# Optimization experiments

Hardware: AMD Instinct MI355X
Metric: run time of the kernel (lower is better)

Reference implementation:

```python
import jax, jax.numpy as jnp
import numpy as np

N_NODE = 200000
EMB = 64
N_EDGES = 2000000
LAYERS = 3
EPS_NORM = 1e-12


def setup_inputs() -> dict:
    key = jax.random.key(0)
    ks = jax.random.split(key, 13)
    d = EMB
    return {
        "user_emb": jax.random.normal(ks[0], (N_NODE, d), jnp.float32),
        "W0": jax.random.normal(ks[1], (d, d), jnp.float32) * np.float32(np.sqrt(2.0 / d)),
        "b0": jax.random.normal(ks[2], (1, d), jnp.float32) * 0.1,
        "W1": jax.random.normal(ks[3], (d, d), jnp.float32) * np.float32(np.sqrt(2.0 / d)),
        "b1": jax.random.normal(ks[4], (1, d), jnp.float32) * 0.1,
        "att": jax.random.normal(ks[5], (1, d), jnp.float32) * 0.1,
        "att_m": jax.random.normal(ks[6], (d, d), jnp.float32) * np.float32(np.sqrt(2.0 / d)),
        "item_rows": jax.random.randint(ks[7], (N_EDGES,), 0, N_NODE, jnp.int32),
        "item_cols": jax.random.randint(ks[8], (N_EDGES,), 0, N_NODE, jnp.int32),
        "item_vals": jax.random.uniform(ks[9], (N_EDGES,), jnp.float32),
        "user_rows": jax.random.randint(ks[10], (N_EDGES,), 0, N_NODE, jnp.int32),
        "user_cols": jax.random.randint(ks[11], (N_EDGES,), 0, N_NODE, jnp.int32),
        "user_vals": jax.random.uniform(ks[12], (N_EDGES,), jnp.float32),
    }


def _spmm(rows, cols, vals, x):
    # y[i] = sum_{edges (i,j)} vals * x[j]   (torch.sparse.mm equivalent)
    gathered = vals[:, None] * x[cols]  # [E, d]
    return jax.ops.segment_sum(gathered, rows, num_segments=N_NODE)


def _l2norm_rows(x):
    # F.normalize(x, p=2, dim=1)
    n = jnp.sqrt(jnp.sum(x * x, axis=1, keepdims=True))
    return x / jnp.maximum(n, EPS_NORM)


def _self_gating(em, W, b):
    return em * jax.nn.sigmoid(em @ W + b)


def _propagate(rows, cols, vals, u):
    acc = u
    for _ in range(LAYERS):
        u = _spmm(rows, cols, vals, u)
        acc = acc + _l2norm_rows(u)
    return acc


def reference(user_emb, W0, b0, W1, b1, att, att_m,
              item_rows, item_cols, item_vals,
              user_rows, user_cols, user_vals):
    u_c2 = _self_gating(user_emb, W0, b0)
    u_c3 = _self_gating(user_emb, W1, b1)
    e2 = _propagate(item_rows, item_cols, item_vals, u_c2)  # [N, d]
    e3 = _propagate(user_rows, user_cols, user_vals, u_c3)  # [N, d]
    # channel attention: per-node scalar score for each channel
    w2 = jnp.sum(att * (e2 @ att_m), axis=1)  # [N]
    w3 = jnp.sum(att * (e3 @ att_m), axis=1)  # [N]
    score = jax.nn.softmax(jnp.stack([w2, w3], axis=1), axis=-1)  # [N, 2]
    mixed = score[:, 0:1] * e2 + score[:, 1:2] * e3  # [N, d]
    return mixed, score
```

## Files before the change

kernel.cpp:

```cpp
#include <hip/hip_runtime.h>

#define N_NODE 200000
#define EMB 64
#define N_EDGES 2000000
#define NROWS_TOTAL (2 * N_NODE)
#define TOT_E (2 * N_EDGES)

#define BSHIFT 9
#define BROWS 512
#define NBUCK ((NROWS_TOTAL + BROWS - 1) / BROWS)
#define NB 1024
#define CHUNK ((TOT_E + NB - 1) / NB)
#define SCAN_N (NBUCK * NB)
#define MAXH 6144

typedef unsigned short bfu;
typedef __attribute__((ext_vector_type(8))) short bf16x8;
typedef __attribute__((ext_vector_type(4))) float f32x4;

__device__ __forceinline__ float bf2f(bfu u) { return __uint_as_float(((unsigned)u) << 16); }
__device__ __forceinline__ bfu f2bf(float f) {
    unsigned b = __float_as_uint(f);
    return (bfu)((b + 0x7FFF + ((b >> 16) & 1)) >> 16);
}

__global__ void gate_kernel(const float* __restrict__ emb,
                            const float* __restrict__ W,
                            const float* __restrict__ b,
                            bfu* __restrict__ out, int n) {
    int t = threadIdx.x;
    int w = t >> 6, lane = t & 63;
    int l16 = lane & 15, kg = lane >> 4;
    bf16x8 Bf[2][4];
#pragma unroll
    for (int kb = 0; kb < 2; ++kb)
#pragma unroll
        for (int nt = 0; nt < 4; ++nt) {
            bf16x8 f;
#pragma unroll
            for (int e = 0; e < 8; ++e)
                f[e] = (short)f2bf(W[(kb * 32 + kg * 8 + e) * 64 + nt * 16 + l16]);
            Bf[kb][nt] = f;
        }
    float bias[4];
#pragma unroll
    for (int nt = 0; nt < 4; ++nt) bias[nt] = b[nt * 16 + l16];
    const float4* e4 = (const float4*)emb;
#pragma unroll 1
    for (int it = 0; it < 4; ++it) {
        int tile = blockIdx.x * 16 + w * 4 + it;
        if (tile * 16 >= n) break;
        int arow = tile * 16 + l16;
        size_t ab = (size_t)arow * 16 + kg * 2;
        float4 a0 = e4[ab], a1 = e4[ab + 1];
        float4 a2 = e4[ab + 8], a3 = e4[ab + 9];
        bf16x8 A0, A1;
        A0[0] = (short)f2bf(a0.x); A0[1] = (short)f2bf(a0.y);
        A0[2] = (short)f2bf(a0.z); A0[3] = (short)f2bf(a0.w);
        A0[4] = (short)f2bf(a1.x); A0[5] = (short)f2bf(a1.y);
        A0[6] = (short)f2bf(a1.z); A0[7] = (short)f2bf(a1.w);
        A1[0] = (short)f2bf(a2.x); A1[1] = (short)f2bf(a2.y);
        A1[2] = (short)f2bf(a2.z); A1[3] = (short)f2bf(a2.w);
        A1[4] = (short)f2bf(a3.x); A1[5] = (short)f2bf(a3.y);
        A1[6] = (short)f2bf(a3.z); A1[7] = (short)f2bf(a3.w);
        f32x4 acc[4];
#pragma unroll
        for (int nt = 0; nt < 4; ++nt) {
            acc[nt] = (f32x4){0.f, 0.f, 0.f, 0.f};
            acc[nt] = __builtin_amdgcn_mfma_f32_16x16x32_bf16(A0, Bf[0][nt], acc[nt], 0, 0, 0);
            acc[nt] = __builtin_amdgcn_mfma_f32_16x16x32_bf16(A1, Bf[1][nt], acc[nt], 0, 0, 0);
        }
#pragma unroll
        for (int nt = 0; nt < 4; ++nt) {
#pragma unroll
            for (int r = 0; r < 4; ++r) {
                int orow = tile * 16 + kg * 4 + r;
                int col = nt * 16 + l16;
                float s = acc[nt][r] + bias[nt];
                float g = 1.0f / (1.0f + __expf(-s));
                float xv = emb[(size_t)orow * 64 + col];
                out[(size_t)orow * 64 + col] = f2bf(xv * g);
            }
        }
    }
}

__global__ void binA_kernel(const int* __restrict__ item_rows,
                            const int* __restrict__ user_rows,
                            int* __restrict__ bc) {
    __shared__ int h[NBUCK];
    int t = threadIdx.x, blk = blockIdx.x;
    for (int k = t; k < NBUCK; k += 256) h[k] = 0;
    __syncthreads();
    int lo = blk * CHUNK, hi = min(lo + CHUNK, TOT_E);
    for (int i = lo + t; i < hi; i += 256) {
        int g = (i < N_EDGES) ? item_rows[i] : (N_NODE + user_rows[i - N_EDGES]);
        atomicAdd(&h[g >> BSHIFT], 1);
    }
    __syncthreads();
    for (int k = t; k < NBUCK; k += 256) bc[k * NB + blk] = h[k];
}

__global__ void scan1_kernel(const int* __restrict__ bc, int* __restrict__ bsumP,
                             int* __restrict__ btot) {
    int b = blockIdx.x, t = threadIdx.x;
    int base = b * NB + t * 4;
    int sR = 0, sP = 0;
#pragma unroll
    for (int k = 0; k < 4; ++k) {
        int c = bc[base + k];
        sR += c;
        sP += (c + 7) & ~7;
    }
#pragma unroll
    for (int off = 32; off; off >>= 1) {
        sR += __shfl_xor(sR, off);
        sP += __shfl_xor(sP, off);
    }
    __shared__ int wsR[4], wsP[4];
    int lane = t & 63, w = t >> 6;
    if (lane == 0) { wsR[w] = sR; wsP[w] = sP; }
    __syncthreads();
    if (t == 0) {
        btot[b] = wsR[0] + wsR[1] + wsR[2] + wsR[3];
        bsumP[b] = wsP[0] + wsP[1] + wsP[2] + wsP[3];
    }
}

__global__ void scan2_kernel(const int* __restrict__ bsumP, const int* __restrict__ btot,
                             int* __restrict__ boffP, int* __restrict__ bbase) {
    __shared__ int sh[1024];
    int t = threadIdx.x;
    int vP = (t < NBUCK) ? bsumP[t] : 0;
    sh[t] = vP;
    __syncthreads();
    for (int off = 1; off < 1024; off <<= 1) {
        int u = (t >= off) ? sh[t - off] : 0;
        __syncthreads();
        sh[t] += u;
        __syncthreads();
    }
    if (t < NBUCK) boffP[t] = sh[t] - vP;
    if (t == 1023) boffP[NBUCK] = sh[1023];
    __syncthreads();
    int vR = (t < NBUCK) ? btot[t] : 0;
    sh[t] = vR;
    __syncthreads();
    for (int off = 1; off < 1024; off <<= 1) {
        int u = (t >= off) ? sh[t - off] : 0;
        __syncthreads();
        sh[t] += u;
        __syncthreads();
    }
    if (t < NBUCK) bbase[t] = sh[t] - vR;
}

__global__ void scan3_kernel(const int* __restrict__ bc, const int* __restrict__ boffP,
                             int* __restrict__ soffP) {
    int b = blockIdx.x, t = threadIdx.x;
    int lane = t & 63, w = t >> 6;
    int base = b * NB + t * 4;
    int p[4];
#pragma unroll
    for (int k = 0; k < 4; ++k) p[k] = (bc[base + k] + 7) & ~7;
    int e1 = p[0], e2 = p[0] + p[1], e3 = p[0] + p[1] + p[2];
    int tsum = e3 + p[3];
    int incl = tsum;
#pragma unroll
    for (int off = 1; off < 64; off <<= 1) {
        int u = __shfl_up(incl, off);
        if (lane >= off) incl += u;
    }
    int excl = incl - tsum;
    __shared__ int wsum[4];
    if (lane == 63) wsum[w] = incl;
    __syncthreads();
    int woff = 0;
    for (int k = 0; k < 4; ++k) if (k < w) woff += wsum[k];
    int g = boffP[b] + woff + excl;
    soffP[base + 0] = g;
    soffP[base + 1] = g + e1;
    soffP[base + 2] = g + e2;
    soffP[base + 3] = g + e3;
}

__global__ void binB_kernel(const int* __restrict__ item_rows, const int* __restrict__ item_cols,
                            const float* __restrict__ item_vals,
                            const int* __restrict__ user_rows, const int* __restrict__ user_cols,
                            const float* __restrict__ user_vals,
                            const int* __restrict__ bc, const int* __restrict__ soffP,
                            int2* __restrict__ staged) {
    __shared__ int2 ebuf[CHUNK];
    __shared__ unsigned short sbk[CHUNK];
    __shared__ int lbase[NBUCK + 1];
    __shared__ int lcur[NBUCK];
    __shared__ int gb[NBUCK];
    __shared__ int wsum[4];
    int t = threadIdx.x, blk = blockIdx.x;
    for (int k = t; k < NBUCK; k += 256) gb[k] = soffP[k * NB + blk];
    {
        int i0 = t * 4;
        int p0 = (i0 < NBUCK) ? bc[i0 * NB + blk] : 0;
        int p1 = (i0 + 1 < NBUCK) ? bc[(i0 + 1) * NB + blk] : 0;
        int p2 = (i0 + 2 < NBUCK) ? bc[(i0 + 2) * NB + blk] : 0;
        int p3 = (i0 + 3 < NBUCK) ? bc[(i0 + 3) * NB + blk] : 0;
        int tsum = p0 + p1 + p2 + p3;
        int lane = t & 63, w = t >> 6;
        int incl = tsum;
#pragma unroll
        for (int off = 1; off < 64; off <<= 1) {
            int u = __shfl_up(incl, off);
            if (lane >= off) incl += u;
        }
        if (lane == 63) wsum[w] = incl;
        __syncthreads();
        int woff = 0;
        for (int k = 0; k < w; ++k) woff += wsum[k];
        int excl = woff + incl - tsum;
        if (i0 < NBUCK) { lbase[i0] = excl; lcur[i0] = excl; }
        if (i0 + 1 < NBUCK) { lbase[i0 + 1] = excl + p0; lcur[i0 + 1] = excl + p0; }
        if (i0 + 2 < NBUCK) { lbase[i0 + 2] = excl + p0 + p1; lcur[i0 + 2] = excl + p0 + p1; }
        if (i0 + 3 < NBUCK) { lbase[i0 + 3] = excl + p0 + p1 + p2; lcur[i0 + 3] = excl + p0 + p1 + p2; }
        if (t == 255) lbase[NBUCK] = excl + tsum;
    }
    __syncthreads();
    int lo = blk * CHUNK, hi = min(lo + CHUNK, TOT_E);
    int cnt = hi - lo;
    for (int i = lo + t; i < hi; i += 256) {
        int g, c; float v;
        if (i < N_EDGES) { g = item_rows[i]; c = item_cols[i]; v = item_vals[i]; }
        else { int j = i - N_EDGES; g = N_NODE + user_rows[j]; c = user_cols[j]; v = user_vals[j]; }
        int bk = g >> BSHIFT;
        int s = atomicAdd(&lcur[bk], 1);
        ebuf[s] = make_int2(((g & (BROWS - 1)) << 18) | c, __float_as_int(v));
        sbk[s] = (unsigned short)bk;
    }
    __syncthreads();
    for (int j = t; j < cnt; j += 256) {
        int k = sbk[j];
        staged[gb[k] + (j - lbase[k])] = ebuf[j];
    }
    for (int k = t; k < NBUCK; k += 256) {
        int c = lbase[k + 1] - lbase[k];
        int s = gb[k] + c, e = gb[k] + ((c + 7) & ~7);
        for (int q = s; q < e; ++q) staged[q] = make_int2(-1, 0);
    }
}

__global__ void finalize_kernel(const int2* __restrict__ staged, const int* __restrict__ boffP,
                                const int* __restrict__ bbase,
                                int* __restrict__ row_ptr, int2* __restrict__ ecv) {
    __shared__ int hist[BROWS];
    __shared__ int start[BROWS + 1];
    __shared__ int2 ebuf[MAXH];
    __shared__ int wsum[4];
    int b = blockIdx.x, t = threadIdx.x;
    int base = boffP[b], end = boffP[b + 1];
    int ebase = bbase[b];
    hist[t * 2] = 0; hist[t * 2 + 1] = 0;
    __syncthreads();
    for (int k = base + t; k < end; k += 256) {
        int gx = staged[k].x;
        if (gx >= 0) atomicAdd(&hist[gx >> 18], 1);
    }
    __syncthreads();
    int i0 = t * 2;
    int c0 = hist[i0], c1 = hist[i0 + 1];
    int tsum = c0 + c1;
    int lane = t & 63, w = t >> 6;
    int incl = tsum;
#pragma unroll
    for (int off = 1; off < 64; off <<= 1) {
        int u = __shfl_up(incl, off);
        if (lane >= off) incl += u;
    }
    if (lane == 63) wsum[w] = incl;
    __syncthreads();
    int woff = 0;
    for (int k = 0; k < w; ++k) woff += wsum[k];
    int excl = woff + incl - tsum;
    start[i0] = excl; start[i0 + 1] = excl + c0;
    if (t == 255) start[BROWS] = excl + tsum;
    __syncthreads();
    int tot = start[BROWS];
#pragma unroll
    for (int q = 0; q < 2; ++q) {
        int r = i0 + q;
        int g = (b << BSHIFT) + r;
        if (g < NROWS_TOTAL) row_ptr[g] = ebase + start[r];
    }
    if (b == 0 && t == 0) row_ptr[NROWS_TOTAL] = TOT_E;
    if (tot <= MAXH) {
        hist[i0] = start[i0]; hist[i0 + 1] = start[i0 + 1];
        __syncthreads();
        for (int k = base + t; k < end; k += 256) {
            int2 p = staged[k];
            if (p.x < 0) continue;
            int l = atomicAdd(&hist[p.x >> 18], 1);
            ebuf[l] = make_int2(p.x & 0x3FFFF, p.y);
        }
        __syncthreads();
        for (int j = t; j < tot; j += 256) ecv[ebase + j] = ebuf[j];
    } else {
        hist[i0] = ebase + start[i0]; hist[i0 + 1] = ebase + start[i0 + 1];
        __syncthreads();
        for (int k = base + t; k < end; k += 256) {
            int2 p = staged[k];
            if (p.x < 0) continue;
            int pos = atomicAdd(&hist[p.x >> 18], 1);
            ecv[pos] = make_int2(p.x & 0x3FFFF, p.y);
        }
    }
}

__global__ void spmm_y(const int* __restrict__ row_ptr, const int2* __restrict__ ecv,
                       const bfu* __restrict__ x,
                       bfu* __restrict__ y, float* __restrict__ rinv, int n) {
    int t = threadIdx.x;
    int lane = t & 63;
    int sub = lane >> 4;
    int l16 = lane & 15;
    int i = blockIdx.x * 16 + (t >> 6) * 4 + sub;
    if (i >= n) return;
    int s = row_ptr[i], e = row_ptr[i + 1];
    const ushort4* x4 = (const ushort4*)x;
    float4 a = make_float4(0.f, 0.f, 0.f, 0.f);
    int gbase = sub * 16;
    for (int base = s; base < e; base += 16) {
        int idx = base + l16;
        int cl = 0; float vl = 0.0f;
        if (idx < e) { int2 p = ecv[idx]; cl = p.x; vl = __int_as_float(p.y); }
        int cnt = min(16, e - base);
        int cnt4 = (cnt + 3) & ~3;
        for (int k = 0; k < cnt4; k += 4) {
#pragma unroll
            for (int u = 0; u < 4; ++u) {
                int c = __shfl(cl, gbase + k + u);
                float v = __shfl(vl, gbase + k + u);
                ushort4 xv = x4[(size_t)c * 16 + l16];
                a.x += v * bf2f(xv.x); a.y += v * bf2f(xv.y);
                a.z += v * bf2f(xv.z); a.w += v * bf2f(xv.w);
            }
        }
    }
    size_t o4 = (size_t)i * 16 + l16;
    ushort4 bv;
    bv.x = f2bf(a.x); bv.y = f2bf(a.y); bv.z = f2bf(a.z); bv.w = f2bf(a.w);
    ((ushort4*)y)[o4] = bv;
    float sq = a.x * a.x + a.y * a.y + a.z * a.z + a.w * a.w;
#pragma unroll
    for (int off = 8; off; off >>= 1) sq += __shfl_xor(sq, off);
    if (l16 == 0) rinv[i] = 1.0f / fmaxf(sqrtf(sq), 1e-12f);
}

__global__ void spmm_sum(const int* __restrict__ row_ptr, const int2* __restrict__ ecv,
                         const bfu* __restrict__ x ,
                         const bfu* __restrict__ u0, const bfu* __restrict__ y1,
                         const float* __restrict__ r1, const float* __restrict__ r2,
                         float* __restrict__ mixed, int n) {
    int t = threadIdx.x;
    int lane = t & 63;
    int sub = lane >> 4;
    int l16 = lane & 15;
    int i = blockIdx.x * 16 + (t >> 6) * 4 + sub;
    if (i >= n) return;
    int s = row_ptr[i], e = row_ptr[i + 1];
    const ushort4* x4 = (const ushort4*)x;
    float4 a = make_float4(0.f, 0.f, 0.f, 0.f);
    int gbase = sub * 16;
    for (int base = s; base < e; base += 16) {
        int idx = base + l16;
        int cl = 0; float vl = 0.0f;
        if (idx < e) { int2 p = ecv[idx]; cl = p.x; vl = __int_as_float(p.y); }
        int cnt = min(16, e - base);
        int cnt4 = (cnt + 3) & ~3;
        for (int k = 0; k < cnt4; k += 4) {
#pragma unroll
            for (int u = 0; u < 4; ++u) {
                int c = __shfl(cl, gbase + k + u);
                float v = __shfl(vl, gbase + k + u);
                ushort4 xv = x4[(size_t)c * 16 + l16];
                a.x += v * bf2f(xv.x); a.y += v * bf2f(xv.y);
                a.z += v * bf2f(xv.z); a.w += v * bf2f(xv.w);
            }
        }
    }
    float sq = a.x * a.x + a.y * a.y + a.z * a.z + a.w * a.w;
#pragma unroll
    for (int off = 8; off; off >>= 1) sq += __shfl_xor(sq, off);
    float r3 = 1.0f / fmaxf(sqrtf(sq), 1e-12f);
    size_t o4 = (size_t)i * 16 + l16;
    float a1 = r1[i], a2 = r2[i];
    ushort4 b0 = ((const ushort4*)u0)[o4];
    ushort4 b1 = ((const ushort4*)y1)[o4];
    ushort4 b2 = ((const ushort4*)x)[o4];
    float4 o;
    o.x = bf2f(b0.x) + a1 * bf2f(b1.x) + a2 * bf2f(b2.x) + r3 * a.x;
    o.y = bf2f(b0.y) + a1 * bf2f(b1.y) + a2 * bf2f(b2.y) + r3 * a.y;
    o.z = bf2f(b0.z) + a1 * bf2f(b1.z) + a2 * bf2f(b2.z) + r3 * a.z;
    o.w = bf2f(b0.w) + a1 * bf2f(b1.w) + a2 * bf2f(b2.w) + r3 * a.w;
    ((float4*)mixed)[o4] = o;
}

__global__ void spmm_mix(const int* __restrict__ row_ptr, const int2* __restrict__ ecv,
                         const bfu* __restrict__ x ,
                         const bfu* __restrict__ u0, const bfu* __restrict__ y1,
                         const float* __restrict__ r1, const float* __restrict__ r2,
                         float* __restrict__ mixed, const float* __restrict__ vvec,
                         float* __restrict__ score, int n) {
    int t = threadIdx.x;
    int lane = t & 63;
    int sub = lane >> 4;
    int l16 = lane & 15;
    int i = blockIdx.x * 16 + (t >> 6) * 4 + sub;
    if (i >= n) return;
    int s = row_ptr[i], e = row_ptr[i + 1];
    const ushort4* x4 = (const ushort4*)x;
    float4 a = make_float4(0.f, 0.f, 0.f, 0.f);
    int gbase = sub * 16;
    for (int base = s; base < e; base += 16) {
        int idx = base + l16;
        int cl = 0; float vl = 0.0f;
        if (idx < e) { int2 p = ecv[idx]; cl = p.x; vl = __int_as_float(p.y); }
        int cnt = min(16, e - base);
        int cnt4 = (cnt + 3) & ~3;
        for (int k = 0; k < cnt4; k += 4) {
#pragma unroll
            for (int u = 0; u < 4; ++u) {
                int c = __shfl(cl, gbase + k + u);
                float v = __shfl(vl, gbase + k + u);
                ushort4 xv = x4[(size_t)c * 16 + l16];
                a.x += v * bf2f(xv.x); a.y += v * bf2f(xv.y);
                a.z += v * bf2f(xv.z); a.w += v * bf2f(xv.w);
            }
        }
    }
    float sq = a.x * a.x + a.y * a.y + a.z * a.z + a.w * a.w;
#pragma unroll
    for (int off = 8; off; off >>= 1) sq += __shfl_xor(sq, off);
    float r3 = 1.0f / fmaxf(sqrtf(sq), 1e-12f);
    size_t o4 = (size_t)i * 16 + l16;
    float a1 = r1[i], a2s = r2[i];
    ushort4 b0 = ((const ushort4*)u0)[o4];
    ushort4 b1 = ((const ushort4*)y1)[o4];
    ushort4 b2 = ((const ushort4*)x)[o4];
    float4 a3;
    a3.x = bf2f(b0.x) + a1 * bf2f(b1.x) + a2s * bf2f(b2.x) + r3 * a.x;
    a3.y = bf2f(b0.y) + a1 * bf2f(b1.y) + a2s * bf2f(b2.y) + r3 * a.y;
    a3.z = bf2f(b0.z) + a1 * bf2f(b1.z) + a2s * bf2f(b2.z) + r3 * a.z;
    a3.w = bf2f(b0.w) + a1 * bf2f(b1.w) + a2s * bf2f(b2.w) + r3 * a.w;
    float4 a2 = ((float4*)mixed)[o4];
    float4 vv = ((const float4*)vvec)[l16];
    float w2 = a2.x * vv.x + a2.y * vv.y + a2.z * vv.z + a2.w * vv.w;
    float w3 = a3.x * vv.x + a3.y * vv.y + a3.z * vv.z + a3.w * vv.w;
#pragma unroll
    for (int off = 8; off; off >>= 1) {
        w2 += __shfl_xor(w2, off);
        w3 += __shfl_xor(w3, off);
    }
    float m = fmaxf(w2, w3);
    float x2 = __expf(w2 - m), x3 = __expf(w3 - m);
    float inv = 1.0f / (x2 + x3);
    float s2 = x2 * inv, s3 = x3 * inv;
    float4 o;
    o.x = s2 * a2.x + s3 * a3.x; o.y = s2 * a2.y + s3 * a3.y;
    o.z = s2 * a2.z + s3 * a3.z; o.w = s2 * a2.w + s3 * a3.w;
    ((float4*)mixed)[o4] = o;
    if (l16 == 0) { score[(size_t)i * 2] = s2; score[(size_t)i * 2 + 1] = s3; }
}

__global__ void vvec_kernel(const float* __restrict__ att_m, const float* __restrict__ att,
                            float* __restrict__ v) {
    int k = threadIdx.x;
    float s = 0.0f;
    for (int j = 0; j < 64; ++j) s += att_m[k * 64 + j] * att[j];
    v[k] = s;
}

extern "C" void kernel_launch(void* const* d_in, const int* in_sizes, int n_in,
                              void* d_out, int out_size, void* d_ws, size_t ws_size,
                              hipStream_t stream) {
    const float* user_emb = (const float*)d_in[0];
    const float* W0 = (const float*)d_in[1];
    const float* b0 = (const float*)d_in[2];
    const float* W1 = (const float*)d_in[3];
    const float* b1 = (const float*)d_in[4];
    const float* att = (const float*)d_in[5];
    const float* att_m = (const float*)d_in[6];
    const int* item_rows = (const int*)d_in[7];
    const int* item_cols = (const int*)d_in[8];
    const float* item_vals = (const float*)d_in[9];
    const int* user_rows = (const int*)d_in[10];
    const int* user_cols = (const int*)d_in[11];
    const float* user_vals = (const float*)d_in[12];

    float* out = (float*)d_out;
    float* mixed = out;
    float* score = out + (size_t)N_NODE * 64;

    char* w = (char*)d_ws;
    bfu* u0 = (bfu*)w;         w += (size_t)N_NODE * 64 * 2;
    bfu* y1 = (bfu*)w;         w += (size_t)N_NODE * 64 * 2;
    bfu* y2 = (bfu*)w;         w += (size_t)N_NODE * 64 * 2;
    float* rv1 = (float*)w;    w += (size_t)N_NODE * 4;
    float* rv2 = (float*)w;    w += (size_t)N_NODE * 4;
    int* row_ptr = (int*)w;    w += ((size_t)NROWS_TOTAL + 64) * 4;
    int2* ecv = (int2*)w;      w += (size_t)TOT_E * 8;
    float* vvec = (float*)w;   w += 256;
    int* bc = (int*)w;         w += (size_t)SCAN_N * 4;
    int* soffP = (int*)w;      w += (size_t)SCAN_N * 4;
    int* bsumP = (int*)w;      w += (NBUCK + 8) * 4;
    int* btot = (int*)w;       w += (NBUCK + 8) * 4;
    int* boffP = (int*)w;      w += (NBUCK + 8) * 4;
    int* bbase = (int*)w;      w += (NBUCK + 8) * 4;
    int2* staged = (int2*)u0;

    const int NB16 = (N_NODE + 15) / 16;
    const int GATE_B = (N_NODE / 16 + 15) / 16;
    const int* rp_item = row_ptr;
    const int* rp_user = row_ptr + N_NODE;

    binA_kernel<<<NB, 256, 0, stream>>>(item_rows, user_rows, bc);
    scan1_kernel<<<NBUCK, 256, 0, stream>>>(bc, bsumP, btot);
    scan2_kernel<<<1, 1024, 0, stream>>>(bsumP, btot, boffP, bbase);
    scan3_kernel<<<NBUCK, 256, 0, stream>>>(bc, boffP, soffP);
    binB_kernel<<<NB, 256, 0, stream>>>(item_rows, item_cols, item_vals,
                                        user_rows, user_cols, user_vals, bc, soffP, staged);
    finalize_kernel<<<NBUCK, 256, 0, stream>>>(staged, boffP, bbase, row_ptr, ecv);
    vvec_kernel<<<1, 64, 0, stream>>>(att_m, att, vvec);

    gate_kernel<<<GATE_B, 256, 0, stream>>>(user_emb, W0, b0, u0, N_NODE);
    spmm_y<<<NB16, 256, 0, stream>>>(rp_item, ecv, u0, y1, rv1, N_NODE);
    spmm_y<<<NB16, 256, 0, stream>>>(rp_item, ecv, y1, y2, rv2, N_NODE);
    spmm_sum<<<NB16, 256, 0, stream>>>(rp_item, ecv, y2, u0, y1, rv1, rv2, mixed, N_NODE);

    gate_kernel<<<GATE_B, 256, 0, stream>>>(user_emb, W1, b1, u0, N_NODE);
    spmm_y<<<NB16, 256, 0, stream>>>(rp_user, ecv, u0, y1, rv1, N_NODE);
    spmm_y<<<NB16, 256, 0, stream>>>(rp_user, ecv, y1, y2, rv2, N_NODE);
    spmm_mix<<<NB16, 256, 0, stream>>>(rp_user, ecv, y2, u0, y1, rv1, rv2,
                                       mixed, vvec, score, N_NODE);
}
```

Measured before the change: 438.5 us.

## Assign one wavefront per row and split edges across four lane groups in SpMM

The SpMM kernels now map one 64-lane wavefront to each row instead of one 16-lane group per row. The four 16-lane groups each process every fourth edge, and their partial sums are then reduced with cross-group shuffles. This shortens the serial chain of dependent gathers per row so more loads are in flight at once. In exchange it launches four times as many blocks, adds reduction shuffles, and leaves lanes idle on rows whose degree is not a multiple of four.

```diff
diff --git a/kernel.cpp b/kernel.cpp
--- a/kernel.cpp
+++ b/kernel.cpp
@@ -318,39 +318,35 @@
                        bfu* __restrict__ y, float* __restrict__ rinv, int n) {
     int t = threadIdx.x;
     int lane = t & 63;
-    int sub = lane >> 4;
+    int eg = lane >> 4;
     int l16 = lane & 15;
-    int i = blockIdx.x * 16 + (t >> 6) * 4 + sub;
+    int i = blockIdx.x * 4 + (t >> 6);
     if (i >= n) return;
     int s = row_ptr[i], e = row_ptr[i + 1];
     const ushort4* x4 = (const ushort4*)x;
     float4 a = make_float4(0.f, 0.f, 0.f, 0.f);
-    int gbase = sub * 16;
-    for (int base = s; base < e; base += 16) {
-        int idx = base + l16;
-        int cl = 0; float vl = 0.0f;
-        if (idx < e) { int2 p = ecv[idx]; cl = p.x; vl = __int_as_float(p.y); }
-        int cnt = min(16, e - base);
-        int cnt4 = (cnt + 3) & ~3;
-        for (int k = 0; k < cnt4; k += 4) {
-#pragma unroll
-            for (int u = 0; u < 4; ++u) {
-                int c = __shfl(cl, gbase + k + u);
-                float v = __shfl(vl, gbase + k + u);
-                ushort4 xv = x4[(size_t)c * 16 + l16];
-                a.x += v * bf2f(xv.x); a.y += v * bf2f(xv.y);
-                a.z += v * bf2f(xv.z); a.w += v * bf2f(xv.w);
-            }
-        }
-    }
-    size_t o4 = (size_t)i * 16 + l16;
-    ushort4 bv;
-    bv.x = f2bf(a.x); bv.y = f2bf(a.y); bv.z = f2bf(a.z); bv.w = f2bf(a.w);
-    ((ushort4*)y)[o4] = bv;
+    for (int base = s; base < e; base += 4) {
+        int idx = base + eg;
+        int c = 0; float v = 0.0f;
+        if (idx < e) { int2 p = ecv[idx]; c = p.x; v = __int_as_float(p.y); }
+        ushort4 xv = x4[(size_t)c * 16 + l16];
+        a.x += v * bf2f(xv.x); a.y += v * bf2f(xv.y);
+        a.z += v * bf2f(xv.z); a.w += v * bf2f(xv.w);
+    }
+#pragma unroll
+    for (int off = 16; off <= 32; off <<= 1) {
+        a.x += __shfl_xor(a.x, off); a.y += __shfl_xor(a.y, off);
+        a.z += __shfl_xor(a.z, off); a.w += __shfl_xor(a.w, off);
+    }
+    if (eg == 0) {
+        ushort4 bv;
+        bv.x = f2bf(a.x); bv.y = f2bf(a.y); bv.z = f2bf(a.z); bv.w = f2bf(a.w);
+        ((ushort4*)y)[(size_t)i * 16 + l16] = bv;
+    }
     float sq = a.x * a.x + a.y * a.y + a.z * a.z + a.w * a.w;
 #pragma unroll
-    for (int off = 8; off; off >>= 1) sq += __shfl_xor(sq, off);
-    if (l16 == 0) rinv[i] = 1.0f / fmaxf(sqrtf(sq), 1e-12f);
+    for (int off = 1; off <= 8; off <<= 1) sq += __shfl_xor(sq, off);
+    if (lane == 0) rinv[i] = 1.0f / fmaxf(sqrtf(sq), 1e-12f);
 }
 
 __global__ void spmm_sum(const int* __restrict__ row_ptr, const int2* __restrict__ ecv,
@@ -360,46 +356,43 @@
                          float* __restrict__ mixed, int n) {
     int t = threadIdx.x;
     int lane = t & 63;
-    int sub = lane >> 4;
+    int eg = lane >> 4;
     int l16 = lane & 15;
-    int i = blockIdx.x * 16 + (t >> 6) * 4 + sub;
+    int i = blockIdx.x * 4 + (t >> 6);
     if (i >= n) return;
     int s = row_ptr[i], e = row_ptr[i + 1];
     const ushort4* x4 = (const ushort4*)x;
     float4 a = make_float4(0.f, 0.f, 0.f, 0.f);
-    int gbase = sub * 16;
-    for (int base = s; base < e; base += 16) {
-        int idx = base + l16;
-        int cl = 0; float vl = 0.0f;
-        if (idx < e) { int2 p = ecv[idx]; cl = p.x; vl = __int_as_float(p.y); }
-        int cnt = min(16, e - base);
-        int cnt4 = (cnt + 3) & ~3;
-        for (int k = 0; k < cnt4; k += 4) {
-#pragma unroll
-            for (int u = 0; u < 4; ++u) {
-                int c = __shfl(cl, gbase + k + u);
-                float v = __shfl(vl, gbase + k + u);
-                ushort4 xv = x4[(size_t)c * 16 + l16];
-                a.x += v * bf2f(xv.x); a.y += v * bf2f(xv.y);
-                a.z += v * bf2f(xv.z); a.w += v * bf2f(xv.w);
-            }
-        }
+    for (int base = s; base < e; base += 4) {
+        int idx = base + eg;
+        int c = 0; float v = 0.0f;
+        if (idx < e) { int2 p = ecv[idx]; c = p.x; v = __int_as_float(p.y); }
+        ushort4 xv = x4[(size_t)c * 16 + l16];
+        a.x += v * bf2f(xv.x); a.y += v * bf2f(xv.y);
+        a.z += v * bf2f(xv.z); a.w += v * bf2f(xv.w);
+    }
+#pragma unroll
+    for (int off = 16; off <= 32; off <<= 1) {
+        a.x += __shfl_xor(a.x, off); a.y += __shfl_xor(a.y, off);
+        a.z += __shfl_xor(a.z, off); a.w += __shfl_xor(a.w, off);
     }
     float sq = a.x * a.x + a.y * a.y + a.z * a.z + a.w * a.w;
 #pragma unroll
-    for (int off = 8; off; off >>= 1) sq += __shfl_xor(sq, off);
-    float r3 = 1.0f / fmaxf(sqrtf(sq), 1e-12f);
-    size_t o4 = (size_t)i * 16 + l16;
-    float a1 = r1[i], a2 = r2[i];
-    ushort4 b0 = ((const ushort4*)u0)[o4];
-    ushort4 b1 = ((const ushort4*)y1)[o4];
-    ushort4 b2 = ((const ushort4*)x)[o4];
-    float4 o;
-    o.x = bf2f(b0.x) + a1 * bf2f(b1.x) + a2 * bf2f(b2.x) + r3 * a.x;
-    o.y = bf2f(b0.y) + a1 * bf2f(b1.y) + a2 * bf2f(b2.y) + r3 * a.y;
-    o.z = bf2f(b0.z) + a1 * bf2f(b1.z) + a2 * bf2f(b2.z) + r3 * a.z;
-    o.w = bf2f(b0.w) + a1 * bf2f(b1.w) + a2 * bf2f(b2.w) + r3 * a.w;
-    ((float4*)mixed)[o4] = o;
+    for (int off = 1; off <= 8; off <<= 1) sq += __shfl_xor(sq, off);
+    if (eg == 0) {
+        float r3 = 1.0f / fmaxf(sqrtf(sq), 1e-12f);
+        size_t o4 = (size_t)i * 16 + l16;
+        float a1 = r1[i], a2 = r2[i];
+        ushort4 b0 = ((const ushort4*)u0)[o4];
+        ushort4 b1 = ((const ushort4*)y1)[o4];
+        ushort4 b2 = ((const ushort4*)x)[o4];
+        float4 o;
+        o.x = bf2f(b0.x) + a1 * bf2f(b1.x) + a2 * bf2f(b2.x) + r3 * a.x;
+        o.y = bf2f(b0.y) + a1 * bf2f(b1.y) + a2 * bf2f(b2.y) + r3 * a.y;
+        o.z = bf2f(b0.z) + a1 * bf2f(b1.z) + a2 * bf2f(b2.z) + r3 * a.z;
+        o.w = bf2f(b0.w) + a1 * bf2f(b1.w) + a2 * bf2f(b2.w) + r3 * a.w;
+        ((float4*)mixed)[o4] = o;
+    }
 }
 
 __global__ void spmm_mix(const int* __restrict__ row_ptr, const int2* __restrict__ ecv,
@@ -410,34 +403,29 @@
                          float* __restrict__ score, int n) {
     int t = threadIdx.x;
     int lane = t & 63;
-    int sub = lane >> 4;
+    int eg = lane >> 4;
     int l16 = lane & 15;
-    int i = blockIdx.x * 16 + (t >> 6) * 4 + sub;
+    int i = blockIdx.x * 4 + (t >> 6);
     if (i >= n) return;
     int s = row_ptr[i], e = row_ptr[i + 1];
     const ushort4* x4 = (const ushort4*)x;
     float4 a = make_float4(0.f, 0.f, 0.f, 0.f);
-    int gbase = sub * 16;
-    for (int base = s; base < e; base += 16) {
-        int idx = base + l16;
-        int cl = 0; float vl = 0.0f;
-        if (idx < e) { int2 p = ecv[idx]; cl = p.x; vl = __int_as_float(p.y); }
-        int cnt = min(16, e - base);
-        int cnt4 = (cnt + 3) & ~3;
-        for (int k = 0; k < cnt4; k += 4) {
-#pragma unroll
-            for (int u = 0; u < 4; ++u) {
-                int c = __shfl(cl, gbase + k + u);
-                float v = __shfl(vl, gbase + k + u);
-                ushort4 xv = x4[(size_t)c * 16 + l16];
-                a.x += v * bf2f(xv.x); a.y += v * bf2f(xv.y);
-                a.z += v * bf2f(xv.z); a.w += v * bf2f(xv.w);
-            }
-        }
+    for (int base = s; base < e; base += 4) {
+        int idx = base + eg;
+        int c = 0; float v = 0.0f;
+        if (idx < e) { int2 p = ecv[idx]; c = p.x; v = __int_as_float(p.y); }
+        ushort4 xv = x4[(size_t)c * 16 + l16];
+        a.x += v * bf2f(xv.x); a.y += v * bf2f(xv.y);
+        a.z += v * bf2f(xv.z); a.w += v * bf2f(xv.w);
+    }
+#pragma unroll
+    for (int off = 16; off <= 32; off <<= 1) {
+        a.x += __shfl_xor(a.x, off); a.y += __shfl_xor(a.y, off);
+        a.z += __shfl_xor(a.z, off); a.w += __shfl_xor(a.w, off);
     }
     float sq = a.x * a.x + a.y * a.y + a.z * a.z + a.w * a.w;
 #pragma unroll
-    for (int off = 8; off; off >>= 1) sq += __shfl_xor(sq, off);
+    for (int off = 1; off <= 8; off <<= 1) sq += __shfl_xor(sq, off);
     float r3 = 1.0f / fmaxf(sqrtf(sq), 1e-12f);
     size_t o4 = (size_t)i * 16 + l16;
     float a1 = r1[i], a2s = r2[i];
@@ -454,7 +442,7 @@
     float w2 = a2.x * vv.x + a2.y * vv.y + a2.z * vv.z + a2.w * vv.w;
     float w3 = a3.x * vv.x + a3.y * vv.y + a3.z * vv.z + a3.w * vv.w;
 #pragma unroll
-    for (int off = 8; off; off >>= 1) {
+    for (int off = 1; off <= 8; off <<= 1) {
         w2 += __shfl_xor(w2, off);
         w3 += __shfl_xor(w3, off);
     }
@@ -462,11 +450,13 @@
     float x2 = __expf(w2 - m), x3 = __expf(w3 - m);
     float inv = 1.0f / (x2 + x3);
     float s2 = x2 * inv, s3 = x3 * inv;
-    float4 o;
-    o.x = s2 * a2.x + s3 * a3.x; o.y = s2 * a2.y + s3 * a3.y;
-    o.z = s2 * a2.z + s3 * a3.z; o.w = s2 * a2.w + s3 * a3.w;
-    ((float4*)mixed)[o4] = o;
-    if (l16 == 0) { score[(size_t)i * 2] = s2; score[(size_t)i * 2 + 1] = s3; }
+    if (eg == 0) {
+        float4 o;
+        o.x = s2 * a2.x + s3 * a3.x; o.y = s2 * a2.y + s3 * a3.y;
+        o.z = s2 * a2.z + s3 * a3.z; o.w = s2 * a2.w + s3 * a3.w;
+        ((float4*)mixed)[o4] = o;
+        if (l16 == 0) { score[(size_t)i * 2] = s2; score[(size_t)i * 2 + 1] = s3; }
+    }
 }
 
 __global__ void vvec_kernel(const float* __restrict__ att_m, const float* __restrict__ att,
@@ -515,7 +505,7 @@
     int* bbase = (int*)w;      w += (NBUCK + 8) * 4;
     int2* staged = (int2*)u0;
 
-    const int NB16 = (N_NODE + 15) / 16;
+    const int NB4 = (N_NODE + 3) / 4;
     const int GATE_B = (N_NODE / 16 + 15) / 16;
     const int* rp_item = row_ptr;
     const int* rp_user = row_ptr + N_NODE;
@@ -530,13 +520,13 @@
     vvec_kernel<<<1, 64, 0, stream>>>(att_m, att, vvec);
 
     gate_kernel<<<GATE_B, 256, 0, stream>>>(user_emb, W0, b0, u0, N_NODE);
-    spmm_y<<<NB16, 256, 0, stream>>>(rp_item, ecv, u0, y1, rv1, N_NODE);
-    spmm_y<<<NB16, 256, 0, stream>>>(rp_item, ecv, y1, y2, rv2, N_NODE);
-    spmm_sum<<<NB16, 256, 0, stream>>>(rp_item, ecv, y2, u0, y1, rv1, rv2, mixed, N_NODE);
+    spmm_y<<<NB4, 256, 0, stream>>>(rp_item, ecv, u0, y1, rv1, N_NODE);
+    spmm_y<<<NB4, 256, 0, stream>>>(rp_item, ecv, y1, y2, rv2, N_NODE);
+    spmm_sum<<<NB4, 256, 0, stream>>>(rp_item, ecv, y2, u0, y1, rv1, rv2, mixed, N_NODE);
 
     gate_kernel<<<GATE_B, 256, 0, stream>>>(user_emb, W1, b1, u0, N_NODE);
-    spmm_y<<<NB16, 256, 0, stream>>>(rp_user, ecv, u0, y1, rv1, N_NODE);
-    spmm_y<<<NB16, 256, 0, stream>>>(rp_user, ecv, y1, y2, rv2, N_NODE);
-    spmm_mix<<<NB16, 256, 0, stream>>>(rp_user, ecv, y2, u0, y1, rv1, rv2,
-                                       mixed, vvec, score, N_NODE);
-}
+    spmm_y<<<NB4, 256, 0, stream>>>(rp_user, ecv, u0, y1, rv1, N_NODE);
+    spmm_y<<<NB4, 256, 0, stream>>>(rp_user, ecv, y1, y2, rv2, N_NODE);
+    spmm_mix<<<NB4, 256, 0, stream>>>(rp_user, ecv, y2, u0, y1, rv1, rv2,
+                                      mixed, vvec, score, N_NODE);
+}
```

Result: slower. 718.1 us (+63.8%).
